# Kernel optimization log

Measured on AMD Instinct MI355X. Metric: run time of the kernel, lower is better.

The kernel has to match this reference:

```python
import jax, jax.numpy as jnp
import numpy as np

EPS = 1e-8
ACT_BITS = 8


def _ternary_vq(t):
    gamma = jnp.abs(t).mean()
    q = jnp.clip(jnp.round(t / (gamma + EPS)), -1.0, 1.0)
    return q * gamma


def setup_inputs() -> dict:
    key = jax.random.key(0)
    k1, k2, k3 = jax.random.split(key, 3)
    in_features, out_features = 1024, 1024
    x = jax.random.normal(k1, (8, 4096, in_features), dtype=jnp.float32)
    weight = jax.random.normal(k2, (out_features, in_features), dtype=jnp.float32)
    bias = jax.random.normal(k3, (out_features,), dtype=jnp.float32)
    return {"x": x, "weight": weight, "bias": bias}


def reference(x, weight, bias):
    # Weight/bias ternary quantization (done once in __init__ of the module)
    wq = _ternary_vq(weight)   # [out, in]
    bq = _ternary_vq(bias)     # [out]

    # Activation quantization: power-of-two scale from global absmax
    qmax = jnp.float32(2 ** (ACT_BITS - 1) - 1)  # 127
    max_val = jnp.max(jnp.abs(x))
    scale = jnp.exp2(jnp.floor(jnp.log2(max_val / qmax + EPS)))
    xq = jnp.round(jnp.clip(x, -qmax * scale, qmax * scale) / scale) * scale

    # F.linear: x @ W^T + b
    return jnp.einsum('bsi,oi->bso', xq, wq) + bq
```

## Files before the change

kernel.cpp:

```cpp
#include <hip/hip_runtime.h>

typedef __attribute__((ext_vector_type(4))) int int4v;

constexpr int Mdim = 32768;
constexpr int Kdim = 1024;
constexpr int Ndim = 1024;
constexpr float FEPS = 1e-8f;

constexpr size_t WQ_OFF = 32768;
constexpr size_t XQ_OFF = WQ_OFF + (size_t)Ndim * Kdim;
constexpr size_t WS_NEED = XQ_OFF + (size_t)Mdim * Kdim;

__device__ __forceinline__ void gload16(const void* g, void* l) {
  __builtin_amdgcn_global_load_lds(
      (const __attribute__((address_space(1))) unsigned int*)g,
      (__attribute__((address_space(3))) unsigned int*)l, 16, 0, 0);
}

__global__ void k_absmax(const uint4* __restrict__ xv, unsigned* __restrict__ pmax, int n4) {
  int i0 = blockIdx.x * blockDim.x + threadIdx.x;
  int stride = gridDim.x * blockDim.x;
  unsigned m = 0u;
  for (int i = i0; i < n4; i += stride) {
    uint4 v = xv[i];
    m = max(m, v.x & 0x7fffffffu);
    m = max(m, v.y & 0x7fffffffu);
    m = max(m, v.z & 0x7fffffffu);
    m = max(m, v.w & 0x7fffffffu);
  }
  #pragma unroll
  for (int off = 32; off > 0; off >>= 1)
    m = max(m, (unsigned)__shfl_down((int)m, off, 64));
  __shared__ unsigned red[4];
  if ((threadIdx.x & 63) == 0) red[threadIdx.x >> 6] = m;
  __syncthreads();
  if (threadIdx.x == 0) {
    unsigned r = max(max(red[0], red[1]), max(red[2], red[3]));
    pmax[blockIdx.x] = r;
  }
}

__global__ void k_wsum(const float4* __restrict__ wv, float* __restrict__ partials, int n4) {
  float s = 0.f;
  int stride = gridDim.x * blockDim.x;
  for (int i = blockIdx.x * blockDim.x + threadIdx.x; i < n4; i += stride) {
    float4 v = wv[i];
    s += fabsf(v.x) + fabsf(v.y) + fabsf(v.z) + fabsf(v.w);
  }
  __shared__ float red[256];
  red[threadIdx.x] = s;
  __syncthreads();
  for (int h = 128; h > 0; h >>= 1) {
    if (threadIdx.x < h) red[threadIdx.x] += red[threadIdx.x + h];
    __syncthreads();
  }
  if (threadIdx.x == 0) partials[blockIdx.x] = red[0];
}

__global__ void k_finalize(const float* __restrict__ bias, const float* __restrict__ partials,
                           const unsigned* __restrict__ pmax,
                           float* __restrict__ scalars, float* __restrict__ bq) {
  __shared__ float redf[256];
  __shared__ unsigned redu[256];
  __shared__ float sh_gb;
  int t = threadIdx.x;

  float s = fabsf(bias[t]) + fabsf(bias[t + 256]) + fabsf(bias[t + 512]) + fabsf(bias[t + 768]);
  redf[t] = s;
  unsigned m = 0u;
  #pragma unroll
  for (int i = 0; i < 8; ++i) m = max(m, pmax[t + 256 * i]);
  redu[t] = m;
  __syncthreads();
  for (int h = 128; h > 0; h >>= 1) {
    if (t < h) {
      redf[t] += redf[t + h];
      redu[t] = max(redu[t], redu[t + h]);
    }
    __syncthreads();
  }
  if (t == 0) {
    float gb = redf[0] / 1024.0f;
    float sw = 0.f;
    for (int i = 0; i < 256; ++i) sw += partials[i];
    float gw = sw / (1024.0f * 1024.0f);
    float maxval = __uint_as_float(redu[0]);
    float v = maxval / 127.0f + FEPS;
    int e = (int)((__float_as_uint(v) >> 23) & 0xff) - 127;
    float scale = ldexpf(1.0f, e);
    scalars[0] = gw;
    scalars[1] = gb;
    scalars[2] = scale;
    scalars[3] = scale * gw;
    scalars[4] = 127.0f * scale;
    scalars[5] = ldexpf(1.0f, -e);
    sh_gb = gb;
  }
  __syncthreads();
  float gb = sh_gb;
  for (int i = t; i < 1024; i += 256) {
    float q = rintf(bias[i] / (gb + FEPS));
    q = fminf(fmaxf(q, -1.0f), 1.0f);
    bq[i] = q * gb;
  }
}

__global__ void k_wquant(const float4* __restrict__ wv, const float* __restrict__ scalars,
                         unsigned* __restrict__ wq, int n4) {
  float inv_g = scalars[0] + FEPS;
  int i0 = blockIdx.x * blockDim.x + threadIdx.x;
  int stride = gridDim.x * blockDim.x;
  for (int i = i0; i < n4; i += stride) {
    float4 v = wv[i];
    int a = (int)rintf(fminf(fmaxf(v.x / inv_g, -1.f), 1.f));
    int b = (int)rintf(fminf(fmaxf(v.y / inv_g, -1.f), 1.f));
    int c = (int)rintf(fminf(fmaxf(v.z / inv_g, -1.f), 1.f));
    int d = (int)rintf(fminf(fmaxf(v.w / inv_g, -1.f), 1.f));
    wq[i] = (unsigned)(a & 0xff) | ((unsigned)(b & 0xff) << 8) |
            ((unsigned)(c & 0xff) << 16) | ((unsigned)(d & 0xff) << 24);
  }
}

__device__ __forceinline__ int qact8(float v, float qs, float inv) {
  return (int)rintf(fminf(fmaxf(v, -qs), qs) * inv);
}

__device__ __forceinline__ unsigned pack4(float4 a, float qs, float inv) {
  return (unsigned)(qact8(a.x, qs, inv) & 0xff) |
         ((unsigned)(qact8(a.y, qs, inv) & 0xff) << 8) |
         ((unsigned)(qact8(a.z, qs, inv) & 0xff) << 16) |
         ((unsigned)(qact8(a.w, qs, inv) & 0xff) << 24);
}

__global__ void k_xquant(const float4* __restrict__ xv, const float* __restrict__ scalars,
                         uint4* __restrict__ xqv, int n16) {
  float qs = scalars[4], inv = scalars[5];
  int i0 = blockIdx.x * blockDim.x + threadIdx.x;
  int stride = gridDim.x * blockDim.x;
  for (int i = i0; i < n16; i += stride) {
    float4 a = xv[4 * i + 0];
    float4 b = xv[4 * i + 1];
    float4 c = xv[4 * i + 2];
    float4 d = xv[4 * i + 3];
    uint4 o;
    o.x = pack4(a, qs, inv);
    o.y = pack4(b, qs, inv);
    o.z = pack4(c, qs, inv);
    o.w = pack4(d, qs, inv);
    xqv[i] = o;
  }
}

__launch_bounds__(256)
__global__ void k_gemm(const unsigned char* __restrict__ xq, const unsigned char* __restrict__ wq,
                       const float* __restrict__ scalars, const float* __restrict__ bq,
                       float* __restrict__ out) {
  __shared__ __align__(16) unsigned char As[128 * 64];
  __shared__ __align__(16) unsigned char Bs[128 * 64];

  const int tid = threadIdx.x;
  const int lane = tid & 63;
  const int wv = tid >> 6;
  const int wr = wv >> 1;
  const int wc = wv & 1;

  int bid = blockIdx.x;
  int swz = (bid & 7) * ((int)gridDim.x >> 3) + (bid >> 3);
  const int mtile = swz >> 3;
  const int ntile = swz & 7;
  const int m0 = mtile * 128;
  const int n0 = ntile * 128;

  int4v acc[4][4];
  #pragma unroll
  for (int i = 0; i < 4; ++i)
    #pragma unroll
    for (int j = 0; j < 4; ++j)
      acc[i][j] = (int4v){0, 0, 0, 0};

  const unsigned char* gA0 = xq + (size_t)(m0 + wv * 32 + (lane >> 2)) * Kdim + (lane & 3) * 16;
  const unsigned char* gB0 = wq + (size_t)(n0 + wv * 32 + (lane >> 2)) * Kdim + (lane & 3) * 16;
  unsigned char* lA0 = As + wv * 2048;
  unsigned char* lA1 = As + wv * 2048 + 1024;
  unsigned char* lB0 = Bs + wv * 2048;
  unsigned char* lB1 = Bs + wv * 2048 + 1024;

  const int fr = lane & 15;
  const int fc = (lane >> 4) * 16;

#define STAGE(kt) do {                              \
    const unsigned char* ga = gA0 + (kt) * 64;      \
    gload16(ga, lA0);                               \
    gload16(ga + 16 * Kdim, lA1);                   \
    const unsigned char* gb = gB0 + (kt) * 64;      \
    gload16(gb, lB0);                               \
    gload16(gb + 16 * Kdim, lB1);                   \
  } while (0)

  STAGE(0);

  for (int kt = 0; kt < Kdim / 64; ++kt) {
    __syncthreads();
    int4v a[4], b[4];
    #pragma unroll
    for (int mi = 0; mi < 4; ++mi)
      a[mi] = *(const int4v*)(As + (wr * 64 + mi * 16 + fr) * 64 + fc);
    #pragma unroll
    for (int ni = 0; ni < 4; ++ni)
      b[ni] = *(const int4v*)(Bs + (wc * 64 + ni * 16 + fr) * 64 + fc);
    #pragma unroll
    for (int mi = 0; mi < 4; ++mi)
      #pragma unroll
      for (int ni = 0; ni < 4; ++ni)
        acc[mi][ni] = __builtin_amdgcn_mfma_i32_16x16x64_i8(a[mi], b[ni], acc[mi][ni], 0, 0, 0);
    __syncthreads();
    if (kt + 1 < Kdim / 64) STAGE(kt + 1);
  }
#undef STAGE

  const float sg = scalars[3];
  #pragma unroll
  for (int ni = 0; ni < 4; ++ni) {
    const int col = n0 + wc * 64 + ni * 16 + fr;
    const float bb = bq[col];
    #pragma unroll
    for (int mi = 0; mi < 4; ++mi) {
      const int rowb = m0 + wr * 64 + mi * 16 + (lane >> 4) * 4;
      #pragma unroll
      for (int r = 0; r < 4; ++r)
        out[(size_t)(rowb + r) * Ndim + col] = (float)acc[mi][ni][r] * sg + bb;
    }
  }
}

extern "C" void kernel_launch(void* const* d_in, const int* in_sizes, int n_in,
                              void* d_out, int out_size, void* d_ws, size_t ws_size,
                              hipStream_t stream) {
  const float* x = (const float*)d_in[0];
  const float* weight = (const float*)d_in[1];
  const float* bias = (const float*)d_in[2];
  float* out = (float*)d_out;

  if (ws_size < WS_NEED) return;

  char* ws = (char*)d_ws;
  float* scalars = (float*)ws;
  float* partials = (float*)(ws + 1024);
  unsigned* pmax = (unsigned*)(ws + 4096);
  float* bq = (float*)(ws + 16384);
  unsigned char* wq = (unsigned char*)(ws + WQ_OFF);
  unsigned char* xq = (unsigned char*)(ws + XQ_OFF);

  k_absmax<<<2048, 256, 0, stream>>>((const uint4*)x, pmax, Mdim * Kdim / 4);
  k_wsum<<<256, 256, 0, stream>>>((const float4*)weight, partials, Ndim * Kdim / 4);
  k_finalize<<<1, 256, 0, stream>>>(bias, partials, pmax, scalars, bq);
  k_wquant<<<512, 256, 0, stream>>>((const float4*)weight, scalars, (unsigned*)wq, Ndim * Kdim / 4);
  k_xquant<<<2048, 256, 0, stream>>>((const float4*)x, scalars, (uint4*)xq, Mdim * Kdim / 16);
  k_gemm<<<2048, 256, 0, stream>>>(xq, wq, scalars, bq, out);
}
```

Baseline: 117.6 us.

## Pre-swizzle int8 operands into MFMA fragment layout and drop LDS staging

The quantize kernels now write x and weight in a blocked layout where each 16-row by 64-k tile is stored in MFMA fragment order, so each lane's 16 bytes are contiguous. The GEMM loads its A/B fragments directly from global memory with register double buffering, removing the LDS tiles and both __syncthreads per k-step. The risk is losing LDS reuse: each fragment is now read from global/L2 by both waves that share it, which raises cache traffic. The quant kernels also now issue 16-byte strided reads per lane instead of plain linear streaming.

Measured after the change: 118.6 us. About the same (+0.9%).

```diff
diff --git a/kernel.cpp b/kernel.cpp
--- a/kernel.cpp
+++ b/kernel.cpp
@@ -10,12 +10,6 @@
 constexpr size_t WQ_OFF = 32768;
 constexpr size_t XQ_OFF = WQ_OFF + (size_t)Ndim * Kdim;
 constexpr size_t WS_NEED = XQ_OFF + (size_t)Mdim * Kdim;
-
-__device__ __forceinline__ void gload16(const void* g, void* l) {
-  __builtin_amdgcn_global_load_lds(
-      (const __attribute__((address_space(1))) unsigned int*)g,
-      (__attribute__((address_space(3))) unsigned int*)l, 16, 0, 0);
-}
 
 __global__ void k_absmax(const uint4* __restrict__ xv, unsigned* __restrict__ pmax, int n4) {
   int i0 = blockIdx.x * blockDim.x + threadIdx.x;
@@ -105,59 +99,62 @@
   }
 }
 
-__global__ void k_wquant(const float4* __restrict__ wv, const float* __restrict__ scalars,
-                         unsigned* __restrict__ wq, int n4) {
-  float inv_g = scalars[0] + FEPS;
-  int i0 = blockIdx.x * blockDim.x + threadIdx.x;
-  int stride = gridDim.x * blockDim.x;
-  for (int i = i0; i < n4; i += stride) {
-    float4 v = wv[i];
-    int a = (int)rintf(fminf(fmaxf(v.x / inv_g, -1.f), 1.f));
-    int b = (int)rintf(fminf(fmaxf(v.y / inv_g, -1.f), 1.f));
-    int c = (int)rintf(fminf(fmaxf(v.z / inv_g, -1.f), 1.f));
-    int d = (int)rintf(fminf(fmaxf(v.w / inv_g, -1.f), 1.f));
-    wq[i] = (unsigned)(a & 0xff) | ((unsigned)(b & 0xff) << 8) |
-            ((unsigned)(c & 0xff) << 16) | ((unsigned)(d & 0xff) << 24);
-  }
-}
-
 __device__ __forceinline__ int qact8(float v, float qs, float inv) {
   return (int)rintf(fminf(fmaxf(v, -qs), qs) * inv);
 }
 
-__device__ __forceinline__ unsigned pack4(float4 a, float qs, float inv) {
-  return (unsigned)(qact8(a.x, qs, inv) & 0xff) |
-         ((unsigned)(qact8(a.y, qs, inv) & 0xff) << 8) |
-         ((unsigned)(qact8(a.z, qs, inv) & 0xff) << 16) |
-         ((unsigned)(qact8(a.w, qs, inv) & 0xff) << 24);
-}
-
-__global__ void k_xquant(const float4* __restrict__ xv, const float* __restrict__ scalars,
-                         uint4* __restrict__ xqv, int n16) {
+__global__ void k_wquant(const float* __restrict__ w, const float* __restrict__ scalars,
+                         unsigned char* __restrict__ wq) {
+  float inv_g = scalars[0] + FEPS;
+  int wave = (blockIdx.x * blockDim.x + threadIdx.x) >> 6;
+  int lane = threadIdx.x & 63;
+  int nb = wave >> 4;
+  int kt = wave & 15;
+  int r = lane >> 2;
+  int c = lane & 3;
+  const float4* src = (const float4*)(w + (size_t)(nb * 16 + r) * Kdim + kt * 64 + c * 16);
+  unsigned o[4];
+  #pragma unroll
+  for (int v = 0; v < 4; ++v) {
+    float4 f = src[v];
+    int a = (int)rintf(fminf(fmaxf(f.x / inv_g, -1.f), 1.f));
+    int b = (int)rintf(fminf(fmaxf(f.y / inv_g, -1.f), 1.f));
+    int cc = (int)rintf(fminf(fmaxf(f.z / inv_g, -1.f), 1.f));
+    int d = (int)rintf(fminf(fmaxf(f.w / inv_g, -1.f), 1.f));
+    o[v] = (unsigned)(a & 0xff) | ((unsigned)(b & 0xff) << 8) |
+           ((unsigned)(cc & 0xff) << 16) | ((unsigned)(d & 0xff) << 24);
+  }
+  uint4 pk; pk.x = o[0]; pk.y = o[1]; pk.z = o[2]; pk.w = o[3];
+  *(uint4*)(wq + (size_t)wave * 1024 + c * 256 + r * 16) = pk;
+}
+
+__global__ void k_xquant(const float* __restrict__ x, const float* __restrict__ scalars,
+                         unsigned char* __restrict__ xq) {
   float qs = scalars[4], inv = scalars[5];
-  int i0 = blockIdx.x * blockDim.x + threadIdx.x;
-  int stride = gridDim.x * blockDim.x;
-  for (int i = i0; i < n16; i += stride) {
-    float4 a = xv[4 * i + 0];
-    float4 b = xv[4 * i + 1];
-    float4 c = xv[4 * i + 2];
-    float4 d = xv[4 * i + 3];
-    uint4 o;
-    o.x = pack4(a, qs, inv);
-    o.y = pack4(b, qs, inv);
-    o.z = pack4(c, qs, inv);
-    o.w = pack4(d, qs, inv);
-    xqv[i] = o;
-  }
+  int wave = (blockIdx.x * blockDim.x + threadIdx.x) >> 6;
+  int lane = threadIdx.x & 63;
+  int mb = wave >> 4;
+  int kt = wave & 15;
+  int r = lane >> 2;
+  int c = lane & 3;
+  const float4* src = (const float4*)(x + (size_t)(mb * 16 + r) * Kdim + kt * 64 + c * 16);
+  unsigned o[4];
+  #pragma unroll
+  for (int v = 0; v < 4; ++v) {
+    float4 f = src[v];
+    o[v] = (unsigned)(qact8(f.x, qs, inv) & 0xff) |
+           ((unsigned)(qact8(f.y, qs, inv) & 0xff) << 8) |
+           ((unsigned)(qact8(f.z, qs, inv) & 0xff) << 16) |
+           ((unsigned)(qact8(f.w, qs, inv) & 0xff) << 24);
+  }
+  uint4 pk; pk.x = o[0]; pk.y = o[1]; pk.z = o[2]; pk.w = o[3];
+  *(uint4*)(xq + (size_t)wave * 1024 + c * 256 + r * 16) = pk;
 }
 
 __launch_bounds__(256)
 __global__ void k_gemm(const unsigned char* __restrict__ xq, const unsigned char* __restrict__ wq,
                        const float* __restrict__ scalars, const float* __restrict__ bq,
                        float* __restrict__ out) {
-  __shared__ __align__(16) unsigned char As[128 * 64];
-  __shared__ __align__(16) unsigned char Bs[128 * 64];
-
   const int tid = threadIdx.x;
   const int lane = tid & 63;
   const int wv = tid >> 6;
@@ -171,6 +168,9 @@
   const int m0 = mtile * 128;
   const int n0 = ntile * 128;
 
+  const unsigned char* Abase = xq + ((size_t)(m0 / 16 + wr * 4) * 16) * 1024 + lane * 16;
+  const unsigned char* Bbase = wq + ((size_t)(n0 / 16 + wc * 4) * 16) * 1024 + lane * 16;
+
   int4v acc[4][4];
   #pragma unroll
   for (int i = 0; i < 4; ++i)
@@ -178,47 +178,38 @@
     for (int j = 0; j < 4; ++j)
       acc[i][j] = (int4v){0, 0, 0, 0};
 
-  const unsigned char* gA0 = xq + (size_t)(m0 + wv * 32 + (lane >> 2)) * Kdim + (lane & 3) * 16;
-  const unsigned char* gB0 = wq + (size_t)(n0 + wv * 32 + (lane >> 2)) * Kdim + (lane & 3) * 16;
-  unsigned char* lA0 = As + wv * 2048;
-  unsigned char* lA1 = As + wv * 2048 + 1024;
-  unsigned char* lB0 = Bs + wv * 2048;
-  unsigned char* lB1 = Bs + wv * 2048 + 1024;
-
+  int4v a0[4], b0[4], a1[4], b1[4];
+
+#define LOADF(abuf, bbuf, kt) do {                                            \
+    _Pragma("unroll")                                                         \
+    for (int mi = 0; mi < 4; ++mi)                                            \
+      abuf[mi] = *(const int4v*)(Abase + ((size_t)mi * 16 + (kt)) * 1024);    \
+    _Pragma("unroll")                                                         \
+    for (int ni = 0; ni < 4; ++ni)                                            \
+      bbuf[ni] = *(const int4v*)(Bbase + ((size_t)ni * 16 + (kt)) * 1024);    \
+  } while (0)
+
+#define MFMAS(abuf, bbuf) do {                                                \
+    _Pragma("unroll")                                                         \
+    for (int mi = 0; mi < 4; ++mi)                                            \
+      _Pragma("unroll")                                                       \
+      for (int ni = 0; ni < 4; ++ni)                                          \
+        acc[mi][ni] = __builtin_amdgcn_mfma_i32_16x16x64_i8(abuf[mi], bbuf[ni], acc[mi][ni], 0, 0, 0); \
+  } while (0)
+
+  LOADF(a0, b0, 0);
+  #pragma unroll
+  for (int kt = 0; kt < 16; kt += 2) {
+    if (kt + 1 < 16) LOADF(a1, b1, kt + 1);
+    MFMAS(a0, b0);
+    if (kt + 2 < 16) LOADF(a0, b0, kt + 2);
+    MFMAS(a1, b1);
+  }
+#undef LOADF
+#undef MFMAS
+
+  const float sg = scalars[3];
   const int fr = lane & 15;
-  const int fc = (lane >> 4) * 16;
-
-#define STAGE(kt) do {                              \
-    const unsigned char* ga = gA0 + (kt) * 64;      \
-    gload16(ga, lA0);                               \
-    gload16(ga + 16 * Kdim, lA1);                   \
-    const unsigned char* gb = gB0 + (kt) * 64;      \
-    gload16(gb, lB0);                               \
-    gload16(gb + 16 * Kdim, lB1);                   \
-  } while (0)
-
-  STAGE(0);
-
-  for (int kt = 0; kt < Kdim / 64; ++kt) {
-    __syncthreads();
-    int4v a[4], b[4];
-    #pragma unroll
-    for (int mi = 0; mi < 4; ++mi)
-      a[mi] = *(const int4v*)(As + (wr * 64 + mi * 16 + fr) * 64 + fc);
-    #pragma unroll
-    for (int ni = 0; ni < 4; ++ni)
-      b[ni] = *(const int4v*)(Bs + (wc * 64 + ni * 16 + fr) * 64 + fc);
-    #pragma unroll
-    for (int mi = 0; mi < 4; ++mi)
-      #pragma unroll
-      for (int ni = 0; ni < 4; ++ni)
-        acc[mi][ni] = __builtin_amdgcn_mfma_i32_16x16x64_i8(a[mi], b[ni], acc[mi][ni], 0, 0, 0);
-    __syncthreads();
-    if (kt + 1 < Kdim / 64) STAGE(kt + 1);
-  }
-#undef STAGE
-
-  const float sg = scalars[3];
   #pragma unroll
   for (int ni = 0; ni < 4; ++ni) {
     const int col = n0 + wc * 64 + ni * 16 + fr;
@@ -254,7 +245,7 @@
   k_absmax<<<2048, 256, 0, stream>>>((const uint4*)x, pmax, Mdim * Kdim / 4);
   k_wsum<<<256, 256, 0, stream>>>((const float4*)weight, partials, Ndim * Kdim / 4);
   k_finalize<<<1, 256, 0, stream>>>(bias, partials, pmax, scalars, bq);
-  k_wquant<<<512, 256, 0, stream>>>((const float4*)weight, scalars, (unsigned*)wq, Ndim * Kdim / 4);
-  k_xquant<<<2048, 256, 0, stream>>>((const float4*)x, scalars, (uint4*)xq, Mdim * Kdim / 16);
+  k_wquant<<<256, 256, 0, stream>>>(weight, scalars, wq);
+  k_xquant<<<8192, 256, 0, stream>>>(x, scalars, xq);
   k_gemm<<<2048, 256, 0, stream>>>(xq, wq, scalars, bq, out);
 }
```
